# Optimization experiments

Measured on AMD Instinct MI355X. Metric: run time of the kernel, lower is better.

Reference implementation:

```python
import jax, jax.numpy as jnp
import numpy as np

N = 10000        # nodes
F_IN = 128       # node features (data.num_node_features)
OUT = 16         # out_channels
H = 32           # attention heads
C1 = 4 * OUT     # hidden per-head dim (4*out_channels)
E = 80000        # directed edges
EPS = 1e-5       # BatchNorm eps
NEG = 0.2        # GATConv LeakyReLU negative_slope


def _gat(x, src, dst, W, a_s, a_d, b, n, C):
    # PyG GATConv, shared lin, concat=False (mean over heads)
    h = (x @ W).reshape(n, H, C)                    # [n,H,C]
    e_src = jnp.sum(h * a_s, -1)                    # [n,H] (alpha from x_j)
    e_dst = jnp.sum(h * a_d, -1)                    # [n,H] (alpha from x_i)
    e = jax.nn.leaky_relu(e_src[src] + e_dst[dst], NEG)     # [E',H]
    m = jax.ops.segment_max(e, dst, num_segments=n)         # segment softmax
    p = jnp.exp(e - m[dst])
    z = jax.ops.segment_sum(p, dst, num_segments=n)
    alpha = p / z[dst]
    out = jax.ops.segment_sum(alpha[:, :, None] * h[src], dst, num_segments=n)
    return out.mean(1) + b                          # mean over heads + bias


def _bn(x, g, b, m, v):  # eval-mode BatchNorm1d (running stats)
    return (x - m) * g / jnp.sqrt(v + EPS) + b


def setup_inputs():
    k = jax.random.split(jax.random.key(0), 40)
    rn = lambda i, s, sc=0.1: jax.random.normal(k[i], s, jnp.float32) * sc
    d = {"x": jax.random.normal(k[0], (N, F_IN), jnp.float32),
         "edge_index": jax.random.randint(k[1], (2, E), 0, N, jnp.int32)}
    # 4 GATConv layers
    d.update(W1=rn(2, (F_IN, H * C1)), as1=rn(3, (H, C1)), ad1=rn(4, (H, C1)), b1=rn(5, (C1,)))
    d.update(W2=rn(6, (C1, H * OUT)), as2=rn(7, (H, OUT)), ad2=rn(8, (H, OUT)), b2=rn(9, (OUT,)))
    d.update(W3=rn(10, (F_IN, H * C1)), as3=rn(11, (H, C1)), ad3=rn(12, (H, C1)), b3=rn(13, (C1,)))
    d.update(W4=rn(14, (C1, H * OUT)), as4=rn(15, (H, OUT)), ad4=rn(16, (H, OUT)), b4=rn(17, (OUT,)))
    # ResidualNetwork(1 block): 1x1 Conv1d over L=1 == matmul
    d.update(rwa=rn(18, (F_IN, OUT)), rba=rn(19, (OUT,)),
             bn1g=jnp.ones(OUT), bn1b=jnp.zeros(OUT), bn1m=rn(20, (OUT,)), bn1v=jnp.abs(rn(21, (OUT,))) + 1.0,
             rwb=rn(22, (OUT, OUT)), rbb=rn(23, (OUT,)),
             bn2g=jnp.ones(OUT), bn2b=jnp.zeros(OUT), bn2m=rn(24, (OUT,)), bn2v=jnp.abs(rn(25, (OUT,))) + 1.0,
             wsc=rn(26, (F_IN, OUT)), bsc=rn(27, (OUT,)),
             bnsg=jnp.ones(OUT), bnsb=jnp.zeros(OUT), bnsm=rn(28, (OUT,)), bnsv=jnp.abs(rn(29, (OUT,))) + 1.0,
             wfc=rn(30, (OUT, OUT)), bfc=rn(31, (OUT,)))
    return d


def reference(x, edge_index, W1, as1, ad1, b1, W2, as2, ad2, b2,
              W3, as3, ad3, b3, W4, as4, ad4, b4,
              rwa, rba, bn1g, bn1b, bn1m, bn1v, rwb, rbb, bn2g, bn2b, bn2m, bn2v,
              wsc, bsc, bnsg, bnsb, bnsm, bnsv, wfc, bfc):
    n = x.shape[0]
    loops = jnp.arange(n, dtype=edge_index.dtype)  # add_self_loops=True
    s2t_src = jnp.concatenate([edge_index[0], loops])  # flow source_to_target
    s2t_dst = jnp.concatenate([edge_index[1], loops])
    t2s_src = jnp.concatenate([edge_index[1], loops])  # flow target_to_source
    t2s_dst = jnp.concatenate([edge_index[0], loops])
    # dropout in original is unassigned (no-op); eval mode assumed
    x_s = jax.nn.elu(_gat(x, s2t_src, s2t_dst, W1, as1, ad1, b1, n, C1))
    x_in = jax.nn.elu(_gat(x_s, s2t_src, s2t_dst, W2, as2, ad2, b2, n, OUT))
    x_t = jax.nn.elu(_gat(x, t2s_src, t2s_dst, W3, as3, ad3, b3, n, C1))
    x_out = jax.nn.elu(_gat(x_t, t2s_src, t2s_dst, W4, as4, ad4, b4, n, OUT))
    # ResidualNetwork: block + identity avg-pool (L=1) + fc
    h = jax.nn.relu(_bn(x @ rwa + rba, bn1g, bn1b, bn1m, bn1v))
    h = _bn(h @ rwb + rbb, bn2g, bn2b, bn2m, bn2v)
    sc = _bn(x @ wsc + bsc, bnsg, bnsb, bnsm, bnsv)
    x_self = jax.nn.relu(h + sc) @ wfc + bfc
    return (x_in, x_out, x_self)
```

## Files before the change

### kernel.cpp

```cpp
#include <hip/hip_runtime.h>
#include <stdint.h>

__device__ __forceinline__ float bf2f(unsigned short u) {
  union { unsigned int i; float f; } v; v.i = ((unsigned int)u) << 16; return v.f;
}
__device__ __forceinline__ unsigned short f2bf(float f) {
  union { float f; unsigned int i; } v; v.f = f;
  unsigned int i = v.i;
  unsigned int r = (i + 0x7fffu + ((i >> 16) & 1u)) >> 16;
  return (unsigned short)r;
}

typedef __bf16 bf16x8 __attribute__((ext_vector_type(8)));
typedef float f32x4 __attribute__((ext_vector_type(4)));
typedef float f32x2 __attribute__((ext_vector_type(2)));
union ABfrag { int4 i4; bf16x8 v; };

#if __has_builtin(__builtin_amdgcn_cvt_pk_fp8_f32) && __has_builtin(__builtin_amdgcn_cvt_pk_f32_fp8)
#define HW_FP8 1
#else
#define HW_FP8 0
#endif

__device__ __forceinline__ unsigned char f2fp8_sw(float f) {
  union { float f; unsigned int u; } v; v.f = f;
  unsigned int s = (v.u >> 24) & 0x80;
  float a = fabsf(f);
  if (a >= 448.f) return (unsigned char)(s | 0x7E);
  v.f = a;
  int ex = (int)(v.u >> 23);
  unsigned int man = v.u & 0x7FFFFFu;
  if (ex >= 121) {
    unsigned int val = ((unsigned int)(ex - 120) << 3) | (man >> 20);
    unsigned int rem = man & 0xFFFFFu;
    if (rem > 0x80000u || (rem == 0x80000u && (val & 1))) val++;
    if (val > 0x7E) val = 0x7E;
    return (unsigned char)(s | val);
  }
  int q = (int)(a * 512.f + 0.5f);
  if (q > 8) q = 8;
  return (unsigned char)(s | (unsigned int)q);
}
__device__ __forceinline__ float fp8dec_sw(unsigned char c) {
  unsigned int e = (c >> 3) & 15u, m = c & 7u;
  float v;
  if (e) { union { unsigned int u; float f; } x; x.u = ((e + 120) << 23) | (m << 20); v = x.f; }
  else v = (float)m * 0.001953125f;
  return (c & 0x80) ? -v : v;
}
__device__ __forceinline__ unsigned int pack4_fp8(float a0, float a1, float a2, float a3) {
#if HW_FP8
  int dw = __builtin_amdgcn_cvt_pk_fp8_f32(a0, a1, 0, false);
  dw = __builtin_amdgcn_cvt_pk_fp8_f32(a2, a3, dw, true);
  return (unsigned int)dw;
#else
  return (unsigned)f2fp8_sw(a0) | ((unsigned)f2fp8_sw(a1) << 8) |
         ((unsigned)f2fp8_sw(a2) << 16) | ((unsigned)f2fp8_sw(a3) << 24);
#endif
}
__device__ __forceinline__ unsigned int bytesel4(uint4 v, int rr) {
#if __has_builtin(__builtin_amdgcn_perm)
  unsigned s = (unsigned)rr | ((unsigned)(rr + 4) << 8);
  unsigned p01 = __builtin_amdgcn_perm(v.y, v.x, s);
  unsigned p23 = __builtin_amdgcn_perm(v.w, v.z, s);
  return __builtin_amdgcn_perm(p23, p01, 0x05040100u);
#else
  int sh = rr * 8;
  return ((v.x >> sh) & 0xFFu) | (((v.y >> sh) & 0xFFu) << 8) |
         (((v.z >> sh) & 0xFFu) << 16) | (((v.w >> sh) & 0xFFu) << 24);
#endif
}
__device__ __forceinline__ void dec16p(int4 g, f32x2 o[8]) {
#if HW_FP8
  o[0] = __builtin_amdgcn_cvt_pk_f32_fp8(g.x, false);
  o[1] = __builtin_amdgcn_cvt_pk_f32_fp8(g.x, true);
  o[2] = __builtin_amdgcn_cvt_pk_f32_fp8(g.y, false);
  o[3] = __builtin_amdgcn_cvt_pk_f32_fp8(g.y, true);
  o[4] = __builtin_amdgcn_cvt_pk_f32_fp8(g.z, false);
  o[5] = __builtin_amdgcn_cvt_pk_f32_fp8(g.z, true);
  o[6] = __builtin_amdgcn_cvt_pk_f32_fp8(g.w, false);
  o[7] = __builtin_amdgcn_cvt_pk_f32_fp8(g.w, true);
#else
  unsigned int w[4] = {(unsigned)g.x, (unsigned)g.y, (unsigned)g.z, (unsigned)g.w};
#pragma unroll
  for (int d = 0; d < 4; ++d) {
    unsigned int x = w[d];
    o[d * 2 + 0] = (f32x2){fp8dec_sw((unsigned char)(x & 0xFF)),
                           fp8dec_sw((unsigned char)((x >> 8) & 0xFF))};
    o[d * 2 + 1] = (f32x2){fp8dec_sw((unsigned char)((x >> 16) & 0xFF)),
                           fp8dec_sw((unsigned char)((x >> 24) & 0xFF))};
  }
#endif
}

__device__ __forceinline__ float lrelu_clamp(float e) {
  e = (e > 0.f) ? e : 0.2f * e;
  return fminf(e, 80.f);
}

__global__ __launch_bounds__(256) void k_detect(const unsigned int* __restrict__ x, int* flag,
                                                int* __restrict__ degAB, int ndeg2) {
  if (blockIdx.x == 0) {
    __shared__ int cnt;
    if (threadIdx.x == 0) cnt = 0;
    __syncthreads();
    int c = 0;
    for (int i = threadIdx.x; i < 1024; i += 256) {
      unsigned int lo = x[i] & 0xFFFFu;
      int ex = (int)((lo >> 7) & 0xFF);
      if (ex >= 100 && ex <= 140) c++;
    }
    atomicAdd(&cnt, c);
    __syncthreads();
    if (threadIdx.x == 0) flag[0] = (cnt > 600) ? 1 : 0;
    return;
  }
  for (int idx = (blockIdx.x - 1) * 256 + threadIdx.x; idx < ndeg2; idx += 8 * 256) degAB[idx] = 0;
}

struct PrepDesc {
  const void* csrc[32]; float* cdst[32]; int cn[32];
  const void* x; float* xc; unsigned short* xp;
  const void* W1; const void* W2; const void* W3; const void* W4;
  unsigned short* P1; unsigned short* P2; unsigned short* P3; unsigned short* P4;
  int* degAB;
  const int* ei;
  int nxb, xtotal, ctotal, E, nn;
};
__global__ __launch_bounds__(256) void k_prep(PrepDesc d, const int* __restrict__ flag) {
  int isbf = *flag;
  int b = blockIdx.x;
  if (b < d.nxb) {
    int t8 = b * 256 + threadIdx.x;
    int i8 = t8 * 8;
    if (i8 < d.xtotal) {
      float v[8];
      if (isbf) {
        int4 raw = *(const int4*)((const unsigned short*)d.x + i8);
        const unsigned short* u = (const unsigned short*)&raw;
#pragma unroll
        for (int j = 0; j < 8; ++j) v[j] = bf2f(u[j]);
      } else {
        float4 f0 = *(const float4*)((const float*)d.x + i8);
        float4 f1 = *(const float4*)((const float*)d.x + i8 + 4);
        v[0] = f0.x; v[1] = f0.y; v[2] = f0.z; v[3] = f0.w;
        v[4] = f1.x; v[5] = f1.y; v[6] = f1.z; v[7] = f1.w;
      }
      *(float4*)(d.xc + i8)     = (float4){v[0], v[1], v[2], v[3]};
      *(float4*)(d.xc + i8 + 4) = (float4){v[4], v[5], v[6], v[7]};
      int row = i8 >> 7, c0 = i8 & 127;
      int tm = row >> 4, mr = row & 15;
      int s = c0 >> 5, quad = (c0 >> 3) & 3;
      unsigned short o[8];
#pragma unroll
      for (int j = 0; j < 8; ++j) o[j] = f2bf(v[j]);
      size_t idx = (((size_t)tm * 4 + s) * 64 + quad * 16 + mr) * 8;
      *(int4*)(d.xp + idx) = *(const int4*)o;
    }
    return;
  }
  b -= d.nxb;
  if (b < 288) {
    int u = b * 256 + threadIdx.x;
    const void* W; unsigned short* P; int K, N, lu;
    if (u < 32768)      { W = d.W1; P = d.P1; K = 128; N = 2048; lu = u; }
    else if (u < 36864) { W = d.W2; P = d.P2; K = 64;  N = 512;  lu = u - 32768; }
    else if (u < 69632) { W = d.W3; P = d.P3; K = 128; N = 2048; lu = u - 36864; }
    else                { W = d.W4; P = d.P4; K = 64;  N = 512;  lu = u - 69632; }
    int ksteps = K >> 5;
    int g = lu / (ksteps * 64);
    int rem = lu - g * (ksteps * 64);
    int s = rem >> 6, lane = rem & 63;
    int mr = lane & 15, quad = lane >> 4;
    int col = g * 16 + mr;
    int kbase = s * 32 + quad * 8;
#pragma unroll
    for (int j = 0; j < 8; ++j) {
      size_t src = (size_t)(kbase + j) * N + col;
      float v = isbf ? bf2f(((const unsigned short*)W)[src]) : ((const float*)W)[src];
      P[(size_t)lu * 8 + j] = f2bf(v);
    }
    return;
  }
  b -= 288;
  if (b < 4) {
    for (int idx = b * 256 + threadIdx.x; idx < d.ctotal; idx += 4 * 256) {
      int t = 0, off = idx;
      while (off >= d.cn[t]) { off -= d.cn[t]; ++t; }
      float v = isbf ? bf2f(((const unsigned short*)d.csrc[t])[off])
                     : ((const float*)d.csrc[t])[off];
      d.cdst[t][off] = v;
    }
    return;
  }
  b -= 4;
  {
    int e = b * 256 + threadIdx.x;
    if (e < d.E) {
      atomicAdd(&d.degAB[d.ei[d.E + e]], 1);
      atomicAdd(&d.degAB[d.nn + d.ei[e]], 1);
    }
  }
}

__global__ __launch_bounds__(1024) void k_exscan2(const int* __restrict__ degA, const int* __restrict__ degB,
                                                  int* __restrict__ rowA, int* __restrict__ rowB,
                                                  int* __restrict__ colA, int* __restrict__ colB,
                                                  int* __restrict__ curA, int* __restrict__ curB, int n) {
  const int* deg = (blockIdx.x == 0) ? degA : degB;
  int* row = (blockIdx.x == 0) ? rowA : rowB;
  int* colx = (blockIdx.x == 0) ? colA : colB;
  int* curx = (blockIdx.x == 0) ? curA : curB;
  __shared__ int wsum[16], wbase[16];
  __shared__ int carry;
  if (threadIdx.x == 0) carry = 0;
  __syncthreads();
  int lane = threadIdx.x & 63, w = threadIdx.x >> 6;
  int chunks = (n + 1023) >> 10;
  for (int ch = 0; ch < chunks; ++ch) {
    int i = (ch << 10) + threadIdx.x;
    int v = (i < n) ? deg[i] : 0;
    int sc = v;
#pragma unroll
    for (int o = 1; o < 64; o <<= 1) { int t = __shfl_up(sc, o); if (lane >= o) sc += t; }
    if (lane == 63) wsum[w] = sc;
    __syncthreads();
    if (threadIdx.x < 16) {
      int v2 = wsum[threadIdx.x], s2 = v2;
#pragma unroll
      for (int o = 1; o < 16; o <<= 1) { int t = __shfl_up(s2, o); if (lane >= o) s2 += t; }
      wbase[threadIdx.x] = s2 - v2;
      if (threadIdx.x == 15) wsum[15] = s2;
    }
    __syncthreads();
    if (i < n) {
      int rv = carry + wbase[w] + (sc - v) + i;
      row[i] = rv;
      colx[rv] = i;
      curx[i] = rv + 1;
    }
    __syncthreads();
    if (threadIdx.x == 0) carry += wsum[15];
    __syncthreads();
  }
  if (threadIdx.x == 0) row[n] = carry + n;
}

struct AuxDesc {
  int resblks, E;
  const int* ei; int* colA; int* colB; int* curA; int* curB;
  const float* xc;
  const float* rp[20];
  void* outbase; size_t eoff; int n;
  const int* flag;
};
__global__ __launch_bounds__(256) void k_aux(AuxDesc d) {
  __shared__ struct { float xs[16][128]; float ha[16][16]; float tt[16][16]; } sm;
  int b = blockIdx.x;
  if (b < d.resblks) {
    int nodebase = b * 16;
    for (int t = threadIdx.x; t < 16 * 128; t += 256)
      sm.xs[t >> 7][t & 127] = d.xc[(size_t)(nodebase + (t >> 7)) * 128 + (t & 127)];
    __syncthreads();
    int ni = threadIdx.x >> 4, c = threadIdx.x & 15;
    const float* rwa = d.rp[0]; const float* rba = d.rp[1];
    const float* bn1g = d.rp[2]; const float* bn1b = d.rp[3];
    const float* bn1m = d.rp[4]; const float* bn1v = d.rp[5];
    const float* rwb = d.rp[6]; const float* rbb = d.rp[7];
    const float* bn2g = d.rp[8]; const float* bn2b = d.rp[9];
    const float* bn2m = d.rp[10]; const float* bn2v = d.rp[11];
    const float* wsc = d.rp[12]; const float* bsc = d.rp[13];
    const float* bnsg = d.rp[14]; const float* bnsb = d.rp[15];
    const float* bnsm = d.rp[16]; const float* bnsv = d.rp[17];
    const float* wfc = d.rp[18]; const float* bfc = d.rp[19];
    float ya = 0.f, ysc = 0.f;
#pragma unroll 8
    for (int k = 0; k < 128; ++k) {
      float xv = sm.xs[ni][k];
      ya  += xv * rwa[k * 16 + c];
      ysc += xv * wsc[k * 16 + c];
    }
    ya += rba[c]; ysc += bsc[c];
    float s1 = bn1g[c] * rsqrtf(bn1v[c] + 1e-5f);
    ya = (ya - bn1m[c]) * s1 + bn1b[c];
    ya = fmaxf(ya, 0.f);
    float ss = bnsg[c] * rsqrtf(bnsv[c] + 1e-5f);
    ysc = (ysc - bnsm[c]) * ss + bnsb[c];
    sm.ha[ni][c] = ya;
    __syncthreads();
    float h2 = rbb[c];
#pragma unroll
    for (int k = 0; k < 16; ++k) h2 += sm.ha[ni][k] * rwb[k * 16 + c];
    float s2 = bn2g[c] * rsqrtf(bn2v[c] + 1e-5f);
    h2 = (h2 - bn2m[c]) * s2 + bn2b[c];
    sm.tt[ni][c] = fmaxf(h2 + ysc, 0.f);
    __syncthreads();
    float o = bfc[c];
#pragma unroll
    for (int k = 0; k < 16; ++k) o += sm.tt[ni][k] * wfc[k * 16 + c];
    size_t oo = d.eoff + (size_t)(nodebase + ni) * 16 + c;
    if (*d.flag) ((unsigned short*)d.outbase)[oo] = f2bf(o);
    else         ((float*)d.outbase)[oo] = o;
    return;
  }
  b -= d.resblks;
  {
    int e = b * 256 + threadIdx.x;
    if (e < d.E) {
      int s = d.ei[e], dd = d.ei[d.E + e];
      d.colA[atomicAdd(&d.curA[dd], 1)] = s;
      d.colB[atomicAdd(&d.curB[s], 1)] = dd;
    }
  }
}

#define TILE_DW 288
template<int CH, int KSTEPS>
__device__ __forceinline__ void mm_es64_body(int rg, int cg, int MT,
    const unsigned short* __restrict__ Ap, const unsigned short* __restrict__ Bp,
    unsigned char* __restrict__ C, const float* __restrict__ a_s, const float* __restrict__ a_d,
    float* __restrict__ es, float* __restrict__ ed, int N, unsigned int* tile) {
  const int TI = KSTEPS * 64;
  int vt = MT - rg * 4; if (vt > 4) vt = 4;
  int wid = threadIdx.x >> 6;
  int tn = cg * 4 + wid;
  int lane = threadIdx.x & 63;
  int mr = lane & 15, quad = lane >> 4;
  const int4* ap = (const int4*)(Ap + (size_t)rg * 4 * TI * 8) + lane;
  const unsigned short* bp = Bp + ((size_t)tn * 4 * KSTEPS) * 512 + lane * 8;
  unsigned int* twave = tile + wid * TILE_DW;
  f32x4 acc[4][4];
#pragma unroll
  for (int rt = 0; rt < 4; ++rt)
#pragma unroll
    for (int nt = 0; nt < 4; ++nt) acc[rt][nt] = (f32x4){0.f, 0.f, 0.f, 0.f};
#pragma unroll
  for (int s = 0; s < KSTEPS; ++s) {
    ABfrag bfr[4];
#pragma unroll
    for (int nt = 0; nt < 4; ++nt) bfr[nt].i4 = *(const int4*)(bp + (size_t)(nt * KSTEPS + s) * 512);
    ABfrag afr[4];
#pragma unroll
    for (int rt = 0; rt < 4; ++rt) {
      int rti = (rt < vt) ? rt : 0;
      afr[rt].i4 = ap[rti * TI + s * 64];
    }
#pragma unroll
    for (int nt = 0; nt < 4; ++nt)
#pragma unroll
      for (int rt = 0; rt < 4; ++rt)
        acc[rt][nt] = __builtin_amdgcn_mfma_f32_16x16x32_bf16(afr[rt].v, bfr[nt].v, acc[rt][nt], 0, 0, 0);
  }
  int r16 = lane >> 2, seg = lane & 3;
  int qr = r16 >> 2, rr = r16 & 3;
#pragma unroll
  for (int rt = 0; rt < 4; ++rt) {
    if (rt < vt) {
      int tm = rg * 4 + rt;
#pragma unroll
      for (int nt = 0; nt < 4; ++nt) {
        unsigned int dwv = pack4_fp8(acc[rt][nt][0], acc[rt][nt][1], acc[rt][nt][2], acc[rt][nt][3]);
        twave[quad * 72 + nt * 16 + mr] = dwv;
      }
      unsigned int out[4];
#pragma unroll
      for (int w = 0; w < 4; ++w) {
        uint4 v = *(const uint4*)&twave[qr * 72 + seg * 16 + 4 * w];
        out[w] = bytesel4(v, rr);
      }
      *(int4*)(C + (size_t)(tm * 16 + r16) * N + tn * 64 + seg * 16) = *(const int4*)out;
    }
  }
  if (CH == 64) {
    const float* asr = a_s + tn * 64;
    const float* adr = a_d + tn * 64;
    float ws[4], wd[4];
#pragma unroll
    for (int nt = 0; nt < 4; ++nt) { ws[nt] = asr[nt * 16 + mr]; wd[nt] = adr[nt * 16 + mr]; }
#pragma unroll
    for (int rt = 0; rt < 4; ++rt) {
      if (rt < vt) {
        int tm = rg * 4 + rt;
        float pes[4] = {0.f,0.f,0.f,0.f}, ped[4] = {0.f,0.f,0.f,0.f};
#pragma unroll
        for (int nt = 0; nt < 4; ++nt)
#pragma unroll
          for (int r = 0; r < 4; ++r) { pes[r] += acc[rt][nt][r] * ws[nt]; ped[r] += acc[rt][nt][r] * wd[nt]; }
#pragma unroll
        for (int m = 1; m < 16; m <<= 1)
#pragma unroll
          for (int r = 0; r < 4; ++r) {
            pes[r] += __shfl_xor(pes[r], m);
            ped[r] += __shfl_xor(ped[r], m);
          }
        if (mr == 0) {
#pragma unroll
          for (int r = 0; r < 4; ++r) {
            int row = tm * 16 + quad * 4 + r;
            es[row * 32 + tn] = pes[r];
            ed[row * 32 + tn] = ped[r];
          }
        }
      }
    }
  } else {
    float ws[4], wd[4];
#pragma unroll
    for (int nt = 0; nt < 4; ++nt) {
      ws[nt] = a_s[(tn * 4 + nt) * 16 + mr];
      wd[nt] = a_d[(tn * 4 + nt) * 16 + mr];
    }
#pragma unroll
    for (int rt = 0; rt < 4; ++rt) {
      if (rt < vt) {
        int tm = rg * 4 + rt;
        float pes[4][4], ped[4][4];
#pragma unroll
        for (int nt = 0; nt < 4; ++nt)
#pragma unroll
          for (int r = 0; r < 4; ++r) { pes[nt][r] = acc[rt][nt][r] * ws[nt]; ped[nt][r] = acc[rt][nt][r] * wd[nt]; }
#pragma unroll
        for (int m = 1; m < 16; m <<= 1)
#pragma unroll
          for (int nt = 0; nt < 4; ++nt)
#pragma unroll
            for (int r = 0; r < 4; ++r) {
              pes[nt][r] += __shfl_xor(pes[nt][r], m);
              ped[nt][r] += __shfl_xor(ped[nt][r], m);
            }
        if (mr == 0) {
#pragma unroll
          for (int nt = 0; nt < 4; ++nt)
#pragma unroll
            for (int r = 0; r < 4; ++r) {
              int row = tm * 16 + quad * 4 + r;
              es[row * 32 + tn * 4 + nt] = pes[nt][r];
              ed[row * 32 + tn * 4 + nt] = ped[nt][r];
            }
        }
      }
    }
  }
}

struct MMDesc {
  const unsigned short* Ap;
  const unsigned short* B1; const unsigned short* B3;
  unsigned char* C1; unsigned char* C3;
  const float* as1; const float* ad1; const float* as3; const float* ad3;
  float* es1; float* ed1; float* es3; float* ed3;
  int mmblks, mt;
};
__global__ __launch_bounds__(256) void k_mm13(MMDesc d) {
  __shared__ unsigned int tile[4 * TILE_DW];
  int b = blockIdx.x;
  if (b < d.mmblks) {
    mm_es64_body<64,4>(b >> 3, b & 7, d.mt, d.Ap, d.B1, d.C1, d.as1, d.ad1, d.es1, d.ed1, 2048, tile);
    return;
  }
  b -= d.mmblks;
  mm_es64_body<64,4>(b >> 3, b & 7, d.mt, d.Ap, d.B3, d.C3, d.as3, d.ad3, d.es3, d.ed3, 2048, tile);
}

__global__ __launch_bounds__(256) void k_g64(const unsigned char* __restrict__ h1,
                                             const unsigned char* __restrict__ h3,
                                             const float* __restrict__ es1, const float* __restrict__ ed1,
                                             const float* __restrict__ es3, const float* __restrict__ ed3,
                                             const int* __restrict__ rowA, const int* __restrict__ colA,
                                             const int* __restrict__ rowB, const int* __restrict__ colB,
                                             const float* __restrict__ b1, const float* __restrict__ b3,
                                             unsigned short* __restrict__ xsp, unsigned short* __restrict__ xtp,
                                             int n, int gb) {
  int b = blockIdx.x;
  const unsigned char* h; const float *es, *ed, *bias; const int *rowp, *col; unsigned short* outp;
  if (b < gb) { h = h1; es = es1; ed = ed1; rowp = rowA; col = colA; bias = b1; outp = xsp; }
  else { b -= gb; h = h3; es = es3; ed = ed3; rowp = rowB; col = colB; bias = b3; outp = xtp; }
  int wid = threadIdx.x >> 6, lane = threadIdx.x & 63;
  int i = b * 4 + wid;
  if (i >= n) return;
  int hd0 = lane >> 2, hd1 = 16 + hd0;
  float e0 = ed[i * 32 + hd0];
  float e1 = ed[i * 32 + hd1];
  int beg = rowp[i], end = rowp[i + 1];
  int deg = end - beg;
  int colv = (lane < deg) ? col[beg + lane] : 0;
  f32x2 acc0[8], acc1[8];
#pragma unroll
  for (int k = 0; k < 8; ++k) { acc0[k] = (f32x2){0.f, 0.f}; acc1[k] = (f32x2){0.f, 0.f}; }
  float Z0 = 0.f, Z1 = 0.f;
  int s0 = __shfl(colv, 0);
  const int4* hp0 = (const int4*)(h + (size_t)s0 * 2048);
  int4 ng0 = hp0[lane];
  int4 ng1 = hp0[64 + lane];
  float na = es[s0 * 32 + hd0];
  float nb = es[s0 * 32 + hd1];
  for (int j = 0; j < deg; ++j) {
    int4 g0 = ng0, g1 = ng1;
    float ea = na, eb = nb;
    int jn = j + 1;
    if (jn < deg) {
      int sn = (jn < 64) ? __shfl(colv, jn) : col[beg + jn];
      const int4* hq = (const int4*)(h + (size_t)sn * 2048);
      ng0 = hq[lane];
      ng1 = hq[64 + lane];
      na = es[sn * 32 + hd0];
      nb = es[sn * 32 + hd1];
    }
    float q0 = __expf(lrelu_clamp(ea + e0));
    float q1 = __expf(lrelu_clamp(eb + e1));
    Z0 += q0; Z1 += q1;
    f32x2 d0[8], d1[8];
    dec16p(g0, d0); dec16p(g1, d1);
    f32x2 q0v = (f32x2){q0, q0}, q1v = (f32x2){q1, q1};
#pragma unroll
    for (int k = 0; k < 8; ++k) {
      acc0[k] = __builtin_elementwise_fma(q0v, d0[k], acc0[k]);
      acc1[k] = __builtin_elementwise_fma(q1v, d1[k], acc1[k]);
    }
  }
  float zi0 = 1.0f / Z0, zi1 = 1.0f / Z1;
  f32x2 zi0v = (f32x2){zi0, zi0}, zi1v = (f32x2){zi1, zi1};
  f32x2 v2[8];
#pragma unroll
  for (int k = 0; k < 8; ++k)
    v2[k] = __builtin_elementwise_fma(acc1[k], zi1v, acc0[k] * zi0v);
#pragma unroll
  for (int m = 4; m < 64; m <<= 1)
#pragma unroll
    for (int k = 0; k < 8; ++k) {
      v2[k].x += __shfl_xor(v2[k].x, m);
      v2[k].y += __shfl_xor(v2[k].y, m);
    }
  if (lane < 4) {
    float v[16];
#pragma unroll
    for (int k = 0; k < 8; ++k) { v[2 * k] = v2[k].x; v[2 * k + 1] = v2[k].y; }
    int tm = i >> 4, mr = i & 15;
    unsigned short ob[16];
#pragma unroll
    for (int k = 0; k < 16; ++k) {
      float t = v[k] * (1.f / 32.f) + bias[lane * 16 + k];
      t = (t > 0.f) ? t : (__expf(t) - 1.f);
      ob[k] = f2bf(t);
    }
    int s0w = lane >> 1;
#pragma unroll
    for (int g2 = 0; g2 < 2; ++g2) {
      size_t idx = (((size_t)tm * 2 + s0w) * 64 + ((lane & 1) * 2 + g2) * 16 + mr) * 8;
      *(int4*)(outp + idx) = *(const int4*)(ob + g2 * 8);
    }
  }
}

__global__ __launch_bounds__(256) void k_mm24(const unsigned short* __restrict__ xsp,
                                              const unsigned short* __restrict__ xtp,
                                              const unsigned short* __restrict__ W2p,
                                              const unsigned short* __restrict__ W4p,
                                              unsigned char* __restrict__ h2, unsigned char* __restrict__ h4,
                                              const float* __restrict__ as2, const float* __restrict__ ad2,
                                              const float* __restrict__ as4, const float* __restrict__ ad4,
                                              float* __restrict__ es2, float* __restrict__ ed2,
                                              float* __restrict__ es4, float* __restrict__ ed4,
                                              int mmblks, int mt) {
  __shared__ unsigned int tile[4 * TILE_DW];
  int b = blockIdx.x;
  if (b < mmblks)
    mm_es64_body<16,2>(b >> 1, b & 1, mt, xsp, W2p, h2, as2, ad2, es2, ed2, 512, tile);
  else {
    b -= mmblks;
    mm_es64_body<16,2>(b >> 1, b & 1, mt, xtp, W4p, h4, as4, ad4, es4, ed4, 512, tile);
  }
}

__global__ __launch_bounds__(256) void k_g16(const unsigned char* __restrict__ h2,
                                             const unsigned char* __restrict__ h4,
                                             const float* __restrict__ es2, const float* __restrict__ ed2,
                                             const float* __restrict__ es4, const float* __restrict__ ed4,
                                             const int* __restrict__ rowA, const int* __restrict__ colA,
                                             const int* __restrict__ rowB, const int* __restrict__ colB,
                                             const float* __restrict__ b2, const float* __restrict__ b4,
                                             void* __restrict__ outbase, int n, int gb,
                                             const int* __restrict__ flag) {
  int b = blockIdx.x;
  const unsigned char* h; const float *es, *ed, *bias; const int *rowp, *col; size_t eoff;
  if (b < gb) { h = h2; es = es2; ed = ed2; rowp = rowA; col = colA; bias = b2; eoff = 0; }
  else { b -= gb; h = h4; es = es4; ed = ed4; rowp = rowB; col = colB; bias = b4; eoff = (size_t)n * 16; }
  int wid = threadIdx.x >> 6, lane = threadIdx.x & 63;
  int i = b * 4 + wid;
  if (i >= n) return;
  int hh = lane & 31, j2 = lane >> 5;
  float ev = ed[i * 32 + hh];
  int beg = rowp[i], end = rowp[i + 1];
  int deg = end - beg;
  int colv = (lane < deg) ? col[beg + lane] : 0;
  f32x2 acc[8];
#pragma unroll
  for (int k = 0; k < 8; ++k) acc[k] = (f32x2){0.f, 0.f};
  float Z = 0.f;
  int j = j2;
  int4 ng = (int4){0, 0, 0, 0};
  float ne = 0.f;
  if (j < deg) {
    int s = __shfl(colv, j);
    ng = ((const int4*)(h + (size_t)s * 512))[hh];
    ne = es[s * 32 + hh];
  }
  for (; j < deg; j += 2) {
    int4 g = ng; float ee = ne;
    int jn = j + 2;
    if (jn < deg) {
      int sn = (jn < 64) ? __shfl(colv, jn) : col[beg + jn];
      ng = ((const int4*)(h + (size_t)sn * 512))[hh];
      ne = es[sn * 32 + hh];
    }
    float q = __expf(lrelu_clamp(ee + ev));
    Z += q;
    f32x2 d[8];
    dec16p(g, d);
    f32x2 qv = (f32x2){q, q};
#pragma unroll
    for (int k = 0; k < 8; ++k) acc[k] = __builtin_elementwise_fma(qv, d[k], acc[k]);
  }
  Z += __shfl_xor(Z, 32);
  float zi = 1.0f / Z;
  f32x2 ziv = (f32x2){zi, zi};
  f32x2 v2[8];
#pragma unroll
  for (int k = 0; k < 8; ++k) v2[k] = acc[k] * ziv;
#pragma unroll
  for (int m = 1; m < 64; m <<= 1)
#pragma unroll
    for (int k = 0; k < 8; ++k) {
      v2[k].x += __shfl_xor(v2[k].x, m);
      v2[k].y += __shfl_xor(v2[k].y, m);
    }
  if (lane == 0) {
    float v[16];
#pragma unroll
    for (int k = 0; k < 8; ++k) { v[2 * k] = v2[k].x; v[2 * k + 1] = v2[k].y; }
    int isbf = *flag;
    if (isbf) {
      unsigned short ob[16];
#pragma unroll
      for (int k = 0; k < 16; ++k) {
        float t = v[k] * (1.f / 32.f) + bias[k];
        t = (t > 0.f) ? t : (__expf(t) - 1.f);
        ob[k] = f2bf(t);
      }
      unsigned short* o = (unsigned short*)outbase + eoff + (size_t)i * 16;
      *(int4*)o = *(const int4*)ob;
      *(int4*)(o + 8) = *(const int4*)(ob + 8);
    } else {
      float* o = (float*)outbase + eoff + (size_t)i * 16;
#pragma unroll
      for (int k = 0; k < 16; ++k) {
        float t = v[k] * (1.f / 32.f) + bias[k];
        t = (t > 0.f) ? t : (__expf(t) - 1.f);
        o[k] = t;
      }
    }
  }
}

extern "C" void kernel_launch(void* const* d_in, const int* in_sizes, int n_in,
                              void* d_out, int out_size, void* d_ws, size_t ws_size,
                              hipStream_t stream) {
  const int n = in_sizes[0] / 128;
  const int E = in_sizes[1] / 2;
  const int* ei = (const int*)d_in[1];

  char* wsp = (char*)d_ws; size_t off = 0;
  auto alloc = [&](size_t bytes) -> void* {
    void* p = wsp + off; off = (off + bytes + 255) & ~(size_t)255; return p;
  };
  int* flag = (int*)alloc(4);
  float* xc = (float*)alloc((size_t)n * 128 * 4);
  unsigned short* xp = (unsigned short*)alloc((size_t)n * 128 * 2);
  unsigned short* W1p = (unsigned short*)alloc((size_t)2048 * 128 * 2);
  unsigned short* W2p = (unsigned short*)alloc((size_t)512 * 64 * 2);
  unsigned short* W3p = (unsigned short*)alloc((size_t)2048 * 128 * 2);
  unsigned short* W4p = (unsigned short*)alloc((size_t)512 * 64 * 2);
  unsigned char* h1 = (unsigned char*)alloc((size_t)n * 2048);
  unsigned char* h3 = (unsigned char*)alloc((size_t)n * 2048);
  unsigned char* h2 = (unsigned char*)alloc((size_t)n * 512);
  unsigned char* h4 = (unsigned char*)alloc((size_t)n * 512);
  float* es1 = (float*)alloc((size_t)n * 32 * 4);
  float* ed1 = (float*)alloc((size_t)n * 32 * 4);
  float* es3 = (float*)alloc((size_t)n * 32 * 4);
  float* ed3 = (float*)alloc((size_t)n * 32 * 4);
  float* es2 = (float*)alloc((size_t)n * 32 * 4);
  float* ed2 = (float*)alloc((size_t)n * 32 * 4);
  float* es4 = (float*)alloc((size_t)n * 32 * 4);
  float* ed4 = (float*)alloc((size_t)n * 32 * 4);
  unsigned short* xsp = (unsigned short*)alloc((size_t)n * 64 * 2);
  unsigned short* xtp = (unsigned short*)alloc((size_t)n * 64 * 2);
  int* rowA = (int*)alloc((size_t)(n + 1) * 4);
  int* rowB = (int*)alloc((size_t)(n + 1) * 4);
  int* colA = (int*)alloc((size_t)(E + n) * 4);
  int* colB = (int*)alloc((size_t)(E + n) * 4);
  int* degAB = (int*)alloc((size_t)2 * n * 4);
  int* degA = degAB, * degB = degAB + n;
  int* curA = (int*)alloc((size_t)n * 4);
  int* curB = (int*)alloc((size_t)n * 4);

  static const int cidx[32] = {3,4,5, 7,8,9, 11,12,13, 15,16,17,
                               18,19,20,21,22,23,24,25,26,27,28,29,
                               30,31,32,33,34,35,36,37};
  PrepDesc pd;
  float* canon[38] = {nullptr};
  pd.ctotal = 0;
  for (int t = 0; t < 32; ++t) {
    int ii = cidx[t];
    canon[ii] = (float*)alloc((size_t)in_sizes[ii] * 4);
    pd.csrc[t] = d_in[ii];
    pd.cdst[t] = canon[ii];
    pd.cn[t] = in_sizes[ii];
    pd.ctotal += in_sizes[ii];
  }
  pd.x = d_in[0]; pd.xc = xc; pd.xp = xp;
  pd.W1 = d_in[2]; pd.W2 = d_in[6]; pd.W3 = d_in[10]; pd.W4 = d_in[14];
  pd.P1 = W1p; pd.P2 = W2p; pd.P3 = W3p; pd.P4 = W4p;
  pd.degAB = degAB;
  pd.ei = ei;
  pd.nxb = (n * 128 / 8 + 255) / 256;
  pd.xtotal = n * 128;
  pd.E = E;
  pd.nn = n;
  (void)ws_size; (void)n_in; (void)out_size;

  const int degblks = (E + 255) / 256;

  k_detect<<<9, 256, 0, stream>>>((const unsigned int*)d_in[0], flag, degAB, 2 * n);
  k_prep<<<pd.nxb + 288 + 4 + degblks, 256, 0, stream>>>(pd, flag);
  k_exscan2<<<2, 1024, 0, stream>>>(degA, degB, rowA, rowB, colA, colB, curA, curB, n);

  const int mt = n / 16;
  const int nrg = (mt + 3) / 4;
  const int mmblks64 = nrg * 8;
  const int mmblks16 = nrg * 2;
  const int gb = (n + 3) / 4;

  AuxDesc ad;
  ad.resblks = mt; ad.E = E;
  ad.ei = ei; ad.colA = colA; ad.colB = colB; ad.curA = curA; ad.curB = curB;
  ad.xc = xc;
  for (int t = 0; t < 20; ++t) ad.rp[t] = canon[18 + t];
  ad.outbase = d_out; ad.eoff = (size_t)2 * n * 16; ad.n = n; ad.flag = flag;
  k_aux<<<mt + degblks, 256, 0, stream>>>(ad);

  MMDesc md;
  md.Ap = xp; md.B1 = W1p; md.B3 = W3p; md.C1 = h1; md.C3 = h3;
  md.as1 = canon[3]; md.ad1 = canon[4]; md.as3 = canon[11]; md.ad3 = canon[12];
  md.es1 = es1; md.ed1 = ed1; md.es3 = es3; md.ed3 = ed3;
  md.mmblks = mmblks64; md.mt = mt;
  k_mm13<<<2 * mmblks64, 256, 0, stream>>>(md);

  k_g64<<<2 * gb, 256, 0, stream>>>(h1, h3, es1, ed1, es3, ed3,
                                    rowA, colA, rowB, colB,
                                    canon[5], canon[13], xsp, xtp, n, gb);
  k_mm24<<<2 * mmblks16, 256, 0, stream>>>(xsp, xtp, W2p, W4p, h2, h4,
                                           canon[7], canon[8], canon[15], canon[16],
                                           es2, ed2, es4, ed4, mmblks16, mt);
  k_g16<<<2 * gb, 256, 0, stream>>>(h2, h4, es2, ed2, es4, ed4,
                                    rowA, colA, rowB, colB,
                                    canon[9], canon[17], d_out, n, gb, flag);
}
```

Before: 324.3 us.

## Precompute W·a attention projections and compute layer-1/3 logits from x in aux kernel

Folds the attention vectors into the weight matrices (W·a_s, W·a_d per head) in the prep kernel, then computes the layer-1 and layer-3 attention logits directly from fp32 x inside the residual aux kernel. The logit epilogue in the large 64-channel matmul is removed, which takes reductions and shuffles off the critical matmul path. In exchange, aux blocks do an extra 128x32x4 matvec per node, and the logits now use fp32 x instead of the fp8-quantized h, which changes numerics slightly.

```diff
diff --git a/kernel.cpp b/kernel.cpp
--- a/kernel.cpp
+++ b/kernel.cpp
@@ -125,6 +125,8 @@
   unsigned short* P1; unsigned short* P2; unsigned short* P3; unsigned short* P4;
   int* degAB;
   const int* ei;
+  const void* av[4];
+  float* wa[4];
   int nxb, xtotal, ctotal, E, nn;
 };
 __global__ __launch_bounds__(256) void k_prep(PrepDesc d, const int* __restrict__ flag) {
@@ -195,10 +197,40 @@
   }
   b -= 4;
   {
-    int e = b * 256 + threadIdx.x;
-    if (e < d.E) {
-      atomicAdd(&d.degAB[d.ei[d.E + e]], 1);
-      atomicAdd(&d.degAB[d.nn + d.ei[e]], 1);
+    int degblks = (d.E + 255) >> 8;
+    if (b < degblks) {
+      int e = b * 256 + threadIdx.x;
+      if (e < d.E) {
+        atomicAdd(&d.degAB[d.ei[d.E + e]], 1);
+        atomicAdd(&d.degAB[d.nn + d.ei[e]], 1);
+      }
+      return;
+    }
+    b -= degblks;
+  }
+  {
+    const void* W = (b < 2) ? d.W1 : d.W3;
+    const void* A = d.av[b];
+    float* out = d.wa[b];
+    int k = threadIdx.x >> 1;
+    int hb = (threadIdx.x & 1) * 16;
+    const unsigned short* Wb = (const unsigned short*)W;
+    const float* Wf = (const float*)W;
+    const unsigned short* Ab = (const unsigned short*)A;
+    const float* Af = (const float*)A;
+#pragma unroll
+    for (int h16 = 0; h16 < 16; ++h16) {
+      int h = hb + h16;
+      float acc = 0.f;
+      size_t wbase = (size_t)k * 2048 + h * 64;
+      int abase = h * 64;
+#pragma unroll 8
+      for (int c = 0; c < 64; ++c) {
+        float wv = isbf ? bf2f(Wb[wbase + c]) : Wf[wbase + c];
+        float av = isbf ? bf2f(Ab[abase + c]) : Af[abase + c];
+        acc += wv * av;
+      }
+      out[k * 32 + h] = acc;
     }
   }
 }
@@ -251,6 +283,8 @@
   const int* ei; int* colA; int* colB; int* curA; int* curB;
   const float* xc;
   const float* rp[20];
+  const float* wa[4];
+  float* es1; float* ed1; float* es3; float* ed3;
   void* outbase; size_t eoff; int n;
   const int* flag;
 };
@@ -263,6 +297,25 @@
       sm.xs[t >> 7][t & 127] = d.xc[(size_t)(nodebase + (t >> 7)) * 128 + (t & 127)];
     __syncthreads();
     int ni = threadIdx.x >> 4, c = threadIdx.x & 15;
+    {
+      const float* w0 = d.wa[0]; const float* w1 = d.wa[1];
+      const float* w2 = d.wa[2]; const float* w3 = d.wa[3];
+      float a0 = 0.f, a1 = 0.f, a2 = 0.f, a3 = 0.f, a4 = 0.f, a5 = 0.f, a6 = 0.f, a7 = 0.f;
+#pragma unroll 4
+      for (int k = 0; k < 128; ++k) {
+        float xv = sm.xs[ni][k];
+        int o = k * 32 + c;
+        a0 += xv * w0[o]; a1 += xv * w0[o + 16];
+        a2 += xv * w1[o]; a3 += xv * w1[o + 16];
+        a4 += xv * w2[o]; a5 += xv * w2[o + 16];
+        a6 += xv * w3[o]; a7 += xv * w3[o + 16];
+      }
+      int row = nodebase + ni;
+      d.es1[row * 32 + c] = a0; d.es1[row * 32 + c + 16] = a1;
+      d.ed1[row * 32 + c] = a2; d.ed1[row * 32 + c + 16] = a3;
+      d.es3[row * 32 + c] = a4; d.es3[row * 32 + c + 16] = a5;
+      d.ed3[row * 32 + c] = a6; d.ed3[row * 32 + c + 16] = a7;
+    }
     const float* rwa = d.rp[0]; const float* rba = d.rp[1];
     const float* bn1g = d.rp[2]; const float* bn1b = d.rp[3];
     const float* bn1m = d.rp[4]; const float* bn1v = d.rp[5];
@@ -371,39 +424,7 @@
       *(int4*)(C + (size_t)(tm * 16 + r16) * N + tn * 64 + seg * 16) = *(const int4*)out;
     }
   }
-  if (CH == 64) {
-    const float* asr = a_s + tn * 64;
-    const float* adr = a_d + tn * 64;
-    float ws[4], wd[4];
-#pragma unroll
-    for (int nt = 0; nt < 4; ++nt) { ws[nt] = asr[nt * 16 + mr]; wd[nt] = adr[nt * 16 + mr]; }
-#pragma unroll
-    for (int rt = 0; rt < 4; ++rt) {
-      if (rt < vt) {
-        int tm = rg * 4 + rt;
-        float pes[4] = {0.f,0.f,0.f,0.f}, ped[4] = {0.f,0.f,0.f,0.f};
-#pragma unroll
-        for (int nt = 0; nt < 4; ++nt)
-#pragma unroll
-          for (int r = 0; r < 4; ++r) { pes[r] += acc[rt][nt][r] * ws[nt]; ped[r] += acc[rt][nt][r] * wd[nt]; }
-#pragma unroll
-        for (int m = 1; m < 16; m <<= 1)
-#pragma unroll
-          for (int r = 0; r < 4; ++r) {
-            pes[r] += __shfl_xor(pes[r], m);
-            ped[r] += __shfl_xor(ped[r], m);
-          }
-        if (mr == 0) {
-#pragma unroll
-          for (int r = 0; r < 4; ++r) {
-            int row = tm * 16 + quad * 4 + r;
-            es[row * 32 + tn] = pes[r];
-            ed[row * 32 + tn] = ped[r];
-          }
-        }
-      }
-    }
-  } else {
+  if (CH == 16) {
     float ws[4], wd[4];
 #pragma unroll
     for (int nt = 0; nt < 4; ++nt) {
@@ -447,19 +468,17 @@
   const unsigned short* Ap;
   const unsigned short* B1; const unsigned short* B3;
   unsigned char* C1; unsigned char* C3;
-  const float* as1; const float* ad1; const float* as3; const float* ad3;
-  float* es1; float* ed1; float* es3; float* ed3;
   int mmblks, mt;
 };
 __global__ __launch_bounds__(256) void k_mm13(MMDesc d) {
   __shared__ unsigned int tile[4 * TILE_DW];
   int b = blockIdx.x;
   if (b < d.mmblks) {
-    mm_es64_body<64,4>(b >> 3, b & 7, d.mt, d.Ap, d.B1, d.C1, d.as1, d.ad1, d.es1, d.ed1, 2048, tile);
+    mm_es64_body<64,4>(b >> 3, b & 7, d.mt, d.Ap, d.B1, d.C1, nullptr, nullptr, nullptr, nullptr, 2048, tile);
     return;
   }
   b -= d.mmblks;
-  mm_es64_body<64,4>(b >> 3, b & 7, d.mt, d.Ap, d.B3, d.C3, d.as3, d.ad3, d.es3, d.ed3, 2048, tile);
+  mm_es64_body<64,4>(b >> 3, b & 7, d.mt, d.Ap, d.B3, d.C3, nullptr, nullptr, nullptr, nullptr, 2048, tile);
 }
 
 __global__ __launch_bounds__(256) void k_g64(const unsigned char* __restrict__ h1,
@@ -702,6 +721,10 @@
   int* degA = degAB, * degB = degAB + n;
   int* curA = (int*)alloc((size_t)n * 4);
   int* curB = (int*)alloc((size_t)n * 4);
+  float* was1 = (float*)alloc((size_t)128 * 32 * 4);
+  float* wad1 = (float*)alloc((size_t)128 * 32 * 4);
+  float* was3 = (float*)alloc((size_t)128 * 32 * 4);
+  float* wad3 = (float*)alloc((size_t)128 * 32 * 4);
 
   static const int cidx[32] = {3,4,5, 7,8,9, 11,12,13, 15,16,17,
                                18,19,20,21,22,23,24,25,26,27,28,29,
@@ -722,6 +745,8 @@
   pd.P1 = W1p; pd.P2 = W2p; pd.P3 = W3p; pd.P4 = W4p;
   pd.degAB = degAB;
   pd.ei = ei;
+  pd.av[0] = d_in[3]; pd.av[1] = d_in[4]; pd.av[2] = d_in[11]; pd.av[3] = d_in[12];
+  pd.wa[0] = was1; pd.wa[1] = wad1; pd.wa[2] = was3; pd.wa[3] = wad3;
   pd.nxb = (n * 128 / 8 + 255) / 256;
   pd.xtotal = n * 128;
   pd.E = E;
@@ -731,7 +756,7 @@
   const int degblks = (E + 255) / 256;
 
   k_detect<<<9, 256, 0, stream>>>((const unsigned int*)d_in[0], flag, degAB, 2 * n);
-  k_prep<<<pd.nxb + 288 + 4 + degblks, 256, 0, stream>>>(pd, flag);
+  k_prep<<<pd.nxb + 288 + 4 + degblks + 4, 256, 0, stream>>>(pd, flag);
   k_exscan2<<<2, 1024, 0, stream>>>(degA, degB, rowA, rowB, colA, colB, curA, curB, n);
 
   const int mt = n / 16;
@@ -745,13 +770,13 @@
   ad.ei = ei; ad.colA = colA; ad.colB = colB; ad.curA = curA; ad.curB = curB;
   ad.xc = xc;
   for (int t = 0; t < 20; ++t) ad.rp[t] = canon[18 + t];
+  ad.wa[0] = was1; ad.wa[1] = wad1; ad.wa[2] = was3; ad.wa[3] = wad3;
+  ad.es1 = es1; ad.ed1 = ed1; ad.es3 = es3; ad.ed3 = ed3;
   ad.outbase = d_out; ad.eoff = (size_t)2 * n * 16; ad.n = n; ad.flag = flag;
   k_aux<<<mt + degblks, 256, 0, stream>>>(ad);
 
   MMDesc md;
   md.Ap = xp; md.B1 = W1p; md.B3 = W3p; md.C1 = h1; md.C3 = h3;
-  md.as1 = canon[3]; md.ad1 = canon[4]; md.as3 = canon[11]; md.ad3 = canon[12];
-  md.es1 = es1; md.ed1 = ed1; md.es3 = es3; md.ed3 = ed3;
   md.mmblks = mmblks64; md.mt = mt;
   k_mm13<<<2 * mmblks64, 256, 0, stream>>>(md);
 
```

Measured after the change: 462.6 us. 42.6% more time.
